# Kernel tuning notes

Hardware: AMD Instinct MI355X
Metric: run time of the kernel (lower is better)

Reference implementation:

```python
import jax, jax.numpy as jnp
import numpy as np

B, N, D = 64, 4096, 512
ATT = 128


def setup_inputs() -> dict:
    key = jax.random.key(0)
    ks = jax.random.split(key, 7)
    s = lambda fan_in: 1.0 / np.sqrt(fan_in)
    return {
        "v_I": jax.random.normal(ks[0], (B, N, D), dtype=jnp.float32),
        "v_Q": jax.random.normal(ks[1], (B, D), dtype=jnp.float32),
        "W_I": jax.random.normal(ks[2], (D, ATT), dtype=jnp.float32) * s(D),
        "W_Q": jax.random.normal(ks[3], (D, ATT), dtype=jnp.float32) * s(D),
        "b_Q": jnp.zeros((ATT,), dtype=jnp.float32),
        "W_p": jax.random.normal(ks[4], (ATT, 1), dtype=jnp.float32) * s(ATT),
        "b_p": jnp.zeros((1,), dtype=jnp.float32),
    }


def reference(v_I, v_Q, W_I, W_Q, b_Q, W_p, b_p):
    # v_I: [B, N, D], v_Q: [B, D]
    v_I_att = jnp.tanh(jnp.einsum("bnd,da->bna", v_I, W_I))          # [B, N, A]
    v_Q_att = jnp.tanh(v_Q @ W_Q + b_Q)[:, None, :]                  # [B, 1, A]
    h_A = jnp.tanh(v_I_att + v_Q_att)                                # [B, N, A]
    # dropout is identity in inference/reference mode
    p_I = (jnp.einsum("bna,ao->bno", h_A, W_p) + b_p)[..., 0]        # [B, N]
    p_I_output = jax.nn.softmax(p_I, axis=-1)                        # [B, N]
    v_att = jnp.einsum("bn,bnd->bd", p_I_output, v_I)                # [B, D]
    u = v_att + v_Q                                                  # [B, D]
    return (p_I_output, u)
```

## Files before the change

### kernel.cpp

```cpp
#include <hip/hip_runtime.h>
#include <cstdint>
#include <cstddef>

#define B_ 64
#define N_ 4096
#define D_ 512
#define A_ 128

typedef unsigned short u16;
typedef __attribute__((ext_vector_type(8))) short bf16x8;
typedef __attribute__((ext_vector_type(4))) float f32x4;

__device__ __forceinline__ u16 cvt_bf16(float x) {
    unsigned u = __float_as_uint(x);
    return (u16)((u + 0x7FFFu + ((u >> 16) & 1u)) >> 16);
}
__device__ __forceinline__ unsigned pack2_bf16(float a, float b) {
    unsigned ua = __float_as_uint(a), ub = __float_as_uint(b);
    unsigned ra = (ua + 0x7FFFu + ((ua >> 16) & 1u)) >> 16;
    unsigned rb = (ub + 0x7FFFu + ((ub >> 16) & 1u)) >> 16;
    return ra | (rb << 16);
}
__device__ __forceinline__ float fast_tanh(float x) {
    float ax = fabsf(x);
    float e  = __expf(-2.0f * ax);
    float r  = __fdividef(1.0f - e, 1.0f + e);
    return x < 0.0f ? -r : r;
}

__global__ void k_prep(const float* __restrict__ WI, const float* __restrict__ vQ,
                       const float* __restrict__ WQ, const float* __restrict__ bQ,
                       u16* __restrict__ Wbf, float* __restrict__ qatt,
                       float* __restrict__ sums, float* __restrict__ u_raw) {
    const int blk = blockIdx.x, t = threadIdx.x;
    if (blk < 64) {
        #pragma unroll
        for (int i = 0; i < 2; ++i) {
            int item = blk * 256 + i * 128 + t;
            int a  = item & 127;
            int d0 = (item >> 7) << 2;
            ushort4 r;
            r.x = cvt_bf16(WI[(d0 + 0) * A_ + a]);
            r.y = cvt_bf16(WI[(d0 + 1) * A_ + a]);
            r.z = cvt_bf16(WI[(d0 + 2) * A_ + a]);
            r.w = cvt_bf16(WI[(d0 + 3) * A_ + a]);
            *(ushort4*)&Wbf[a * D_ + d0] = r;
        }
    } else {
        const int b = blk - 64;
        __shared__ float sq[D_];
        for (int d = t; d < D_; d += 128) sq[d] = vQ[b * D_ + d];
        __syncthreads();
        float acc = bQ[t];
        #pragma unroll 8
        for (int d = 0; d < D_; ++d) acc += sq[d] * WQ[d * A_ + t];
        qatt[b * A_ + t] = fast_tanh(acc);
        float4 z = {0.f, 0.f, 0.f, 0.f};
        *(float4*)(u_raw + b * D_ + t * 4) = z;
        if (t == 0) sums[b] = 0.0f;
    }
}

__global__ void __launch_bounds__(256)
k_fused(const float* __restrict__ vI, const u16* __restrict__ Wbf,
        const float* __restrict__ qatt, const float* __restrict__ Wp,
        float* __restrict__ wbuf, float* __restrict__ sums,
        float* __restrict__ u_raw) {
    const int b  = blockIdx.y;
    const int n0 = blockIdx.x * 128;
    const int t    = threadIdx.x;
    const int lane = t & 63, wave = t >> 6;
    const int l15  = lane & 15, quad = lane >> 4;

    __shared__ float sw[128];
    __shared__ float wred[4];

    f32x4 acc[2][8];
    #pragma unroll
    for (int mt = 0; mt < 2; ++mt)
        #pragma unroll
        for (int nt = 0; nt < 8; ++nt)
            acc[mt][nt] = (f32x4){0.f, 0.f, 0.f, 0.f};

    const float* a0p = vI + (size_t)(b * N_ + n0 + wave * 32 + l15) * D_ + quad * 8;
    const float* a1p = a0p + 16 * D_;
    const u16* bbase = Wbf + (size_t)l15 * D_ + quad * 8;

    float4 c0a = *(const float4*)(a0p);
    float4 c0b = *(const float4*)(a0p + 4);
    float4 c1a = *(const float4*)(a1p);
    float4 c1b = *(const float4*)(a1p + 4);
    #pragma unroll
    for (int kk = 0; kk < 16; ++kk) {
        float4 n0a, n0b, n1a, n1b;
        if (kk < 15) {
            const int ko = (kk + 1) * 32;
            n0a = *(const float4*)(a0p + ko);
            n0b = *(const float4*)(a0p + ko + 4);
            n1a = *(const float4*)(a1p + ko);
            n1b = *(const float4*)(a1p + ko + 4);
        }
        bf16x8 bfr[8];
        #pragma unroll
        for (int nt = 0; nt < 8; ++nt)
            bfr[nt] = *(const bf16x8*)(bbase + nt * 16 * D_ + kk * 32);
        union { bf16x8 v; unsigned u[4]; } c0, c1;
        c0.u[0] = pack2_bf16(c0a.x, c0a.y);
        c0.u[1] = pack2_bf16(c0a.z, c0a.w);
        c0.u[2] = pack2_bf16(c0b.x, c0b.y);
        c0.u[3] = pack2_bf16(c0b.z, c0b.w);
        c1.u[0] = pack2_bf16(c1a.x, c1a.y);
        c1.u[1] = pack2_bf16(c1a.z, c1a.w);
        c1.u[2] = pack2_bf16(c1b.x, c1b.y);
        c1.u[3] = pack2_bf16(c1b.z, c1b.w);
        bf16x8 af[2] = { c0.v, c1.v };
        #pragma unroll
        for (int mt = 0; mt < 2; ++mt)
            #pragma unroll
            for (int nt = 0; nt < 8; ++nt)
                acc[mt][nt] = __builtin_amdgcn_mfma_f32_16x16x32_bf16(
                    af[mt], bfr[nt], acc[mt][nt], 0, 0, 0);
        c0a = n0a; c0b = n0b; c1a = n1a; c1b = n1b;
    }

    float qa_v[8], wp_v[8];
    #pragma unroll
    for (int nt = 0; nt < 8; ++nt) {
        int a = nt * 16 + l15;
        qa_v[nt] = qatt[b * A_ + a];
        wp_v[nt] = Wp[a];
    }
    float lsum = 0.f;
    #pragma unroll
    for (int mt = 0; mt < 2; ++mt) {
        #pragma unroll
        for (int r = 0; r < 4; ++r) {
            float s = 0.f;
            #pragma unroll
            for (int nt = 0; nt < 8; ++nt) {
                float t1 = fast_tanh(acc[mt][nt][r]);
                float h  = fast_tanh(t1 + qa_v[nt]);
                s += h * wp_v[nt];
            }
            s += __shfl_xor(s, 1, 16);
            s += __shfl_xor(s, 2, 16);
            s += __shfl_xor(s, 4, 16);
            s += __shfl_xor(s, 8, 16);
            float we = __expf(s);
            lsum += we;
            if (l15 == 0) {
                int rloc = wave * 32 + mt * 16 + quad * 4 + r;
                wbuf[(size_t)b * N_ + n0 + rloc] = we;
                sw[rloc] = we;
            }
        }
    }
    lsum += __shfl_xor(lsum, 16, 64);
    lsum += __shfl_xor(lsum, 32, 64);
    if (lane == 0) wred[wave] = lsum;
    __syncthreads();
    if (t == 0) atomicAdd(sums + b, wred[0] + wred[1] + wred[2] + wred[3]);

    const int rr = t >> 7;
    const int c  = t & 127;
    const float4* base = (const float4*)(vI + (size_t)(b * N_ + n0 + rr) * D_) + c;
    float a0 = 0.f, a1 = 0.f, a2 = 0.f, a3 = 0.f;
    #pragma unroll 8
    for (int n = 0; n < 128; n += 2) {
        float4 x = base[n * 128];
        float wn = sw[n + rr];
        a0 += wn * x.x; a1 += wn * x.y; a2 += wn * x.z; a3 += wn * x.w;
    }
    float* ub = u_raw + b * D_ + c * 4;
    atomicAdd(ub + 0, a0);
    atomicAdd(ub + 1, a1);
    atomicAdd(ub + 2, a2);
    atomicAdd(ub + 3, a3);
}

__global__ void __launch_bounds__(256)
k_fin(const float* __restrict__ wbuf, const float* __restrict__ sums,
      const float* __restrict__ u_raw, const float* __restrict__ vQ,
      float* __restrict__ p_out, float* __restrict__ u_out) {
    const int b = blockIdx.x, t = threadIdx.x;
    const float inv = 1.0f / sums[b];
    #pragma unroll
    for (int i = 0; i < 4; ++i) {
        float4 x = *(const float4*)(wbuf + (size_t)b * N_ + i * 1024 + t * 4);
        float4 y = { x.x * inv, x.y * inv, x.z * inv, x.w * inv };
        *(float4*)(p_out + (size_t)b * N_ + i * 1024 + t * 4) = y;
    }
    if (t < 128) {
        float4 ur = *(const float4*)(u_raw + b * D_ + t * 4);
        float4 vq = *(const float4*)(vQ + b * D_ + t * 4);
        float4 o  = { ur.x * inv + vq.x, ur.y * inv + vq.y,
                      ur.z * inv + vq.z, ur.w * inv + vq.w };
        *(float4*)(u_out + b * D_ + t * 4) = o;
    }
}

extern "C" void kernel_launch(void* const* d_in, const int* in_sizes, int n_in,
                              void* d_out, int out_size, void* d_ws, size_t ws_size,
                              hipStream_t stream) {
    const float* vI = (const float*)d_in[0];
    const float* vQ = (const float*)d_in[1];
    const float* WI = (const float*)d_in[2];
    const float* WQ = (const float*)d_in[3];
    const float* bQ = (const float*)d_in[4];
    const float* Wp = (const float*)d_in[5];

    float* out_p = (float*)d_out;
    float* out_u = out_p + (size_t)B_ * N_;

    char* ws = (char*)d_ws;
    u16*   Wbf   = (u16*)ws;
    float* qatt  = (float*)(ws + 131072);
    float* sums  = (float*)(ws + 163840);
    float* u_raw = (float*)(ws + 164864);
    float* wbuf  = (float*)(ws + 295936);

    k_prep<<<128, 128, 0, stream>>>(WI, vQ, WQ, bQ, Wbf, qatt, sums, u_raw);
    k_fused<<<dim3(N_ / 128, B_), 256, 0, stream>>>(vI, Wbf, qatt, Wp,
                                                    wbuf, sums, u_raw);
    k_fin<<<B_, 256, 0, stream>>>(wbuf, sums, u_raw, vQ, out_p, out_u);
}
```

Before: 833.6 us.

## Stage vI and W tiles through LDS via global_load_lds in fused kernel

```diff
diff --git a/kernel.cpp b/kernel.cpp
--- a/kernel.cpp
+++ b/kernel.cpp
@@ -6,6 +6,7 @@
 #define N_ 4096
 #define D_ 512
 #define A_ 128
+#define BK 64
 
 typedef unsigned short u16;
 typedef __attribute__((ext_vector_type(8))) short bf16x8;
@@ -26,6 +27,11 @@
     float e  = __expf(-2.0f * ax);
     float r  = __fdividef(1.0f - e, 1.0f + e);
     return x < 0.0f ? -r : r;
+}
+__device__ __forceinline__ void gl_lds16(const void* g, void* l) {
+    __builtin_amdgcn_global_load_lds(
+        (const __attribute__((address_space(1))) unsigned int*)g,
+        (__attribute__((address_space(3))) unsigned int*)l, 16, 0, 0);
 }
 
 __global__ void k_prep(const float* __restrict__ WI, const float* __restrict__ vQ,
@@ -72,6 +78,8 @@
     const int lane = t & 63, wave = t >> 6;
     const int l15  = lane & 15, quad = lane >> 4;
 
+    __shared__ float sA[128 * BK];
+    __shared__ u16   sB[128 * BK];
     __shared__ float sw[128];
     __shared__ float wred[4];
 
@@ -82,45 +90,51 @@
         for (int nt = 0; nt < 8; ++nt)
             acc[mt][nt] = (f32x4){0.f, 0.f, 0.f, 0.f};
 
-    const float* a0p = vI + (size_t)(b * N_ + n0 + wave * 32 + l15) * D_ + quad * 8;
-    const float* a1p = a0p + 16 * D_;
-    const u16* bbase = Wbf + (size_t)l15 * D_ + quad * 8;
-
-    float4 c0a = *(const float4*)(a0p);
-    float4 c0b = *(const float4*)(a0p + 4);
-    float4 c1a = *(const float4*)(a1p);
-    float4 c1b = *(const float4*)(a1p + 4);
-    #pragma unroll
-    for (int kk = 0; kk < 16; ++kk) {
-        float4 n0a, n0b, n1a, n1b;
-        if (kk < 15) {
-            const int ko = (kk + 1) * 32;
-            n0a = *(const float4*)(a0p + ko);
-            n0b = *(const float4*)(a0p + ko + 4);
-            n1a = *(const float4*)(a1p + ko);
-            n1b = *(const float4*)(a1p + ko + 4);
+    const float* ga = vI + (size_t)(b * N_ + n0) * D_;
+
+    const int a_row  = wave * 32 + (lane >> 4);
+    const float* a_g = ga + (size_t)a_row * D_ + (lane & 15) * 4;
+    float* a_l       = sA + (wave * 32) * BK;
+    const int b_row  = wave * 32 + (lane >> 3);
+    const u16* b_g   = Wbf + (size_t)b_row * D_ + (lane & 7) * 8;
+    u16* b_l         = sB + (wave * 32) * BK;
+
+    for (int kr = 0; kr < 8; ++kr) {
+        const int k0 = kr * BK;
+        #pragma unroll
+        for (int c = 0; c < 8; ++c)
+            gl_lds16(a_g + c * 4 * D_ + k0, a_l + c * 4 * BK);
+        #pragma unroll
+        for (int c = 0; c < 4; ++c)
+            gl_lds16(b_g + c * 8 * D_ + k0, b_l + c * 8 * BK);
+        __syncthreads();
+        #pragma unroll
+        for (int ks = 0; ks < 2; ++ks) {
+            bf16x8 af[2];
+            #pragma unroll
+            for (int mt = 0; mt < 2; ++mt) {
+                const float* ap = sA + (wave * 32 + mt * 16 + l15) * BK + ks * 32 + quad * 8;
+                float4 xa = *(const float4*)ap;
+                float4 xb = *(const float4*)(ap + 4);
+                union { bf16x8 v; unsigned u[4]; } cv;
+                cv.u[0] = pack2_bf16(xa.x, xa.y);
+                cv.u[1] = pack2_bf16(xa.z, xa.w);
+                cv.u[2] = pack2_bf16(xb.x, xb.y);
+                cv.u[3] = pack2_bf16(xb.z, xb.w);
+                af[mt] = cv.v;
+            }
+            bf16x8 bfr[8];
+            #pragma unroll
+            for (int nt = 0; nt < 8; ++nt)
+                bfr[nt] = *(const bf16x8*)(sB + (nt * 16 + l15) * BK + ks * 32 + quad * 8);
+            #pragma unroll
+            for (int mt = 0; mt < 2; ++mt)
+                #pragma unroll
+                for (int nt = 0; nt < 8; ++nt)
+                    acc[mt][nt] = __builtin_amdgcn_mfma_f32_16x16x32_bf16(
+                        af[mt], bfr[nt], acc[mt][nt], 0, 0, 0);
         }
-        bf16x8 bfr[8];
-        #pragma unroll
-        for (int nt = 0; nt < 8; ++nt)
-            bfr[nt] = *(const bf16x8*)(bbase + nt * 16 * D_ + kk * 32);
-        union { bf16x8 v; unsigned u[4]; } c0, c1;
-        c0.u[0] = pack2_bf16(c0a.x, c0a.y);
-        c0.u[1] = pack2_bf16(c0a.z, c0a.w);
-        c0.u[2] = pack2_bf16(c0b.x, c0b.y);
-        c0.u[3] = pack2_bf16(c0b.z, c0b.w);
-        c1.u[0] = pack2_bf16(c1a.x, c1a.y);
-        c1.u[1] = pack2_bf16(c1a.z, c1a.w);
-        c1.u[2] = pack2_bf16(c1b.x, c1b.y);
-        c1.u[3] = pack2_bf16(c1b.z, c1b.w);
-        bf16x8 af[2] = { c0.v, c1.v };
-        #pragma unroll
-        for (int mt = 0; mt < 2; ++mt)
-            #pragma unroll
-            for (int nt = 0; nt < 8; ++nt)
-                acc[mt][nt] = __builtin_amdgcn_mfma_f32_16x16x32_bf16(
-                    af[mt], bfr[nt], acc[mt][nt], 0, 0, 0);
-        c0a = n0a; c0b = n0b; c1a = n1a; c1b = n1b;
+        __syncthreads();
     }
 
     float qa_v[8], wp_v[8];
```

Result: faster. 785.4 us (-5.8%).
